# Kernel tuning notes

Hardware: AMD Instinct MI355X
Metric: run time of the kernel (lower is better)

## Reference

```python
import jax, jax.numpy as jnp
import numpy as np

DIM = 512
HEADS = 8
DIM_HEAD = 64
INNER = HEADS * DIM_HEAD  # 512
TOPK_FRAC = 0.7
SCALE = DIM_HEAD ** -0.5


def setup_inputs() -> dict:
    key = jax.random.key(0)
    k1, k2, k3, k4 = jax.random.split(key, 4)
    B, N = 4, 1024
    x = jax.random.normal(k1, (B, N, DIM), dtype=jnp.float32)
    # nn.Linear(dim, inner*3, bias=False): weight [3*inner, dim]; store transposed for x @ W
    w_qkv = jax.random.normal(k2, (DIM, 3 * INNER), dtype=jnp.float32) * (DIM ** -0.5)
    # to_out Linear(inner, dim) with bias
    w_out = jax.random.normal(k3, (INNER, DIM), dtype=jnp.float32) * (INNER ** -0.5)
    b_out = jax.random.normal(k4, (DIM,), dtype=jnp.float32) * 0.01
    return {"x": x, "w_qkv": w_qkv, "w_out": w_out, "b_out": b_out}


def reference(x, w_qkv, w_out, b_out):
    B, N, _ = x.shape
    H, D = HEADS, DIM_HEAD
    qkv = x @ w_qkv  # [B, N, 3*INNER]
    q, k, v = jnp.split(qkv, 3, axis=-1)
    # 'b n (h d) -> b h n d'
    reshape = lambda t: t.reshape(B, N, H, D).transpose(0, 2, 1, 3)
    q, k, v = reshape(q), reshape(k), reshape(v)
    dots = jnp.einsum('bhid,bhjd->bhij', q, k) * SCALE  # [B, H, N, N]
    # per-row top-k masking (kNN attention)
    kk = int(N * TOPK_FRAC)
    _, idx = jax.lax.top_k(dots, kk)  # [B, H, N, kk]
    bi = jnp.arange(B)[:, None, None, None]
    hi = jnp.arange(H)[None, :, None, None]
    ii = jnp.arange(N)[None, None, :, None]
    mask = jnp.zeros_like(dots).at[bi, hi, ii, idx].set(1.0)
    dots = jnp.where(mask > 0, dots, jnp.float32(-jnp.inf))
    attn = jax.nn.softmax(dots, axis=-1)
    out = jnp.einsum('bhij,bhjd->bhid', attn, v)  # [B, H, N, D]
    out = out.transpose(0, 2, 1, 3).reshape(B, N, H * D)  # 'b h n d -> b n (h d)'
    return out @ w_out + b_out
```

## Files before the change

### kernel.cpp

```cpp
#include <hip/hip_runtime.h>
#include <cstddef>

#define B_      4
#define N_      1024
#define DIM_    512
#define H_      8
#define D_      64
#define INNER_  512
#define TRIPLE_ 1536
#define KK_     716
#define SCALE_  0.125f

typedef short bf16x8 __attribute__((ext_vector_type(8)));
typedef float f32x4  __attribute__((ext_vector_type(4)));
typedef unsigned short ushort_t;
typedef ushort_t us8 __attribute__((ext_vector_type(8)));

__device__ __forceinline__ unsigned short bf16_rne(float f) {
    unsigned u = __float_as_uint(f);
    return (unsigned short)((u + 0x7FFFu + ((u >> 16) & 1u)) >> 16);
}
__device__ __forceinline__ float bf16_f(unsigned short s) {
    return __uint_as_float((unsigned)s << 16);
}
__device__ __forceinline__ unsigned f2key(float f) {
    unsigned u = __float_as_uint(f);
    return u ^ ((u & 0x80000000u) ? 0xFFFFFFFFu : 0x80000000u);
}
__device__ __forceinline__ float key2f(unsigned k) {
    unsigned u = (k & 0x80000000u) ? (k ^ 0x80000000u) : ~k;
    return __uint_as_float(u);
}
__device__ __forceinline__ int wave_count(int lc) {
    int c = __popcll(__ballot(lc & 1));
    c += __popcll(__ballot(lc & 2)) << 1;
    c += __popcll(__ballot(lc & 4)) << 2;
    c += __popcll(__ballot(lc & 8)) << 3;
    c += __popcll(__ballot(lc & 16)) << 4;
    return c;
}
__device__ __forceinline__ int count_ge(const unsigned* key, unsigned kt) {
    int lc = 0;
#pragma unroll
    for (int m = 0; m < 16; ++m) lc += (key[m] >= kt) ? 1 : 0;
    return wave_count(lc);
}
__device__ __forceinline__ unsigned bisect_exact(const unsigned* key,
                                                 bool hlo, bool hhi,
                                                 float tlo, float thi) {
    unsigned klo = hlo ? f2key(tlo) : 0u;
    unsigned khi = hhi ? f2key(thi) : 0xFFFFFFFFu;
    while (khi - klo > 1u) {
        const unsigned km = klo + ((khi - klo) >> 1);
        const int c = count_ge(key, km);
        if (c >= KK_) { klo = km; if (c == KK_) break; }
        else khi = km;
    }
    return klo;
}
__device__ __forceinline__ void topk2(const unsigned* key0, const unsigned* key1,
                                      float mu0, float sg0, float mu1, float sg1,
                                      unsigned& out0, unsigned& out1) {
    bool done0 = false, done1 = false;
    float tlo0 = 0.f, thi0 = 0.f, tlo1 = 0.f, thi1 = 0.f;
    int   clo0 = 0,   chi0 = 0,   clo1 = 0,   chi1 = 0;
    bool  hlo0 = false, hhi0 = false, hlo1 = false, hhi1 = false;
    float t0 = mu0 - 0.52189f * sg0;
    float t1 = mu1 - 0.52189f * sg1;
    unsigned res0 = 0u, res1 = 0u;
    for (int it = 0; it < 10; ++it) {
        if (done0 & done1) break;
        const unsigned kt0 = f2key(t0);
        const unsigned kt1 = f2key(t1);
        int lc0 = 0, lc1 = 0;
#pragma unroll
        for (int m = 0; m < 16; ++m) {
            lc0 += (key0[m] >= kt0) ? 1 : 0;
            lc1 += (key1[m] >= kt1) ? 1 : 0;
        }
        const int c0 = wave_count(lc0);
        const int c1 = wave_count(lc1);
        if (!done0) {
            if (c0 == KK_) { res0 = kt0; done0 = true; }
            else {
                if (c0 > KK_) { tlo0 = t0; clo0 = c0; hlo0 = true; }
                else          { thi0 = t0; chi0 = c0; hhi0 = true; }
                float tn;
                if (hlo0 && hhi0) {
                    tn = tlo0 + (thi0 - tlo0) * ((float)(clo0 - KK_) / (float)(clo0 - chi0));
                } else {
                    const float z    = (t0 - mu0) / sg0;
                    const float dens = fmaxf(408.5f * __expf(-0.5f * z * z) / sg0, 1.f);
                    tn = t0 + (float)(c0 - KK_) / dens;
                }
                if (hlo0 && !(tn > tlo0)) tn = hhi0 ? 0.5f * (tlo0 + thi0) : tlo0 + 0.25f * sg0;
                if (hhi0 && !(tn < thi0)) tn = hlo0 ? 0.5f * (tlo0 + thi0) : thi0 - 0.25f * sg0;
                t0 = tn;
            }
        }
        if (!done1) {
            if (c1 == KK_) { res1 = kt1; done1 = true; }
            else {
                if (c1 > KK_) { tlo1 = t1; clo1 = c1; hlo1 = true; }
                else          { thi1 = t1; chi1 = c1; hhi1 = true; }
                float tn;
                if (hlo1 && hhi1) {
                    tn = tlo1 + (thi1 - tlo1) * ((float)(clo1 - KK_) / (float)(clo1 - chi1));
                } else {
                    const float z    = (t1 - mu1) / sg1;
                    const float dens = fmaxf(408.5f * __expf(-0.5f * z * z) / sg1, 1.f);
                    tn = t1 + (float)(c1 - KK_) / dens;
                }
                if (hlo1 && !(tn > tlo1)) tn = hhi1 ? 0.5f * (tlo1 + thi1) : tlo1 + 0.25f * sg1;
                if (hhi1 && !(tn < thi1)) tn = hlo1 ? 0.5f * (tlo1 + thi1) : thi1 - 0.25f * sg1;
                t1 = tn;
            }
        }
    }
    if (!done0) res0 = bisect_exact(key0, hlo0, hhi0, tlo0, thi0);
    if (!done1) res1 = bisect_exact(key1, hlo1, hhi1, tlo1, thi1);
    out0 = res0;
    out1 = res1;
}
__device__ __forceinline__ void split8(const float* __restrict__ src,
                                       bf16x8& h8, bf16x8& l8) {
    float4 a = *(const float4*)src;
    float4 b = *(const float4*)(src + 4);
    float v[8] = {a.x, a.y, a.z, a.w, b.x, b.y, b.z, b.w};
#pragma unroll
    for (int i = 0; i < 8; ++i) {
        ushort_t hb = bf16_rne(v[i]);
        h8[i] = (short)hb;
        l8[i] = (short)bf16_rne(v[i] - bf16_f(hb));
    }
}

__global__ __launch_bounds__(256) void conv_wT2(const float* __restrict__ Wq,
                                                const float* __restrict__ Wo,
                                                ushort_t* __restrict__ WqTh,
                                                ushort_t* __restrict__ WqTl,
                                                ushort_t* __restrict__ WoTh,
                                                ushort_t* __restrict__ WoTl) {
    __shared__ float tile[32][33];
    const bool isQ = blockIdx.x < 48;
    const int  nb  = (isQ ? blockIdx.x : blockIdx.x - 48) * 32;
    const int  kb  = blockIdx.y * 32;
    const int  Nn  = isQ ? TRIPLE_ : DIM_;
    const float* W = isQ ? Wq : Wo;
    ushort_t* Th   = isQ ? WqTh : WoTh;
    ushort_t* Tl   = isQ ? WqTl : WoTl;
    const int tx = threadIdx.x & 31, ty = threadIdx.x >> 5;
    for (int yy = ty; yy < 32; yy += 8)
        tile[yy][tx] = W[(size_t)(kb + yy) * Nn + nb + tx];
    __syncthreads();
    for (int yy = ty; yy < 32; yy += 8) {
        float v = tile[tx][yy];
        ushort_t hb = bf16_rne(v);
        size_t idx = (size_t)(nb + yy) * DIM_ + kb + tx;
        Th[idx] = hb;
        Tl[idx] = bf16_rne(v - bf16_f(hb));
    }
}

__global__ __launch_bounds__(256) void gemm_qkv_mfma(
    const float* __restrict__ X,
    const ushort_t* __restrict__ Wh, const ushort_t* __restrict__ Wl,
    ushort_t* __restrict__ Qh, ushort_t* __restrict__ Ql,
    ushort_t* __restrict__ Kh, ushort_t* __restrict__ Kl,
    ushort_t* __restrict__ Vt) {
    __shared__ ushort_t stile[4][4608];
    __shared__ ushort_t BshH[2][2048];
    __shared__ ushort_t BshL[2][2048];
    const int t = threadIdx.x, w = t >> 6, l = t & 63;
    const int ln = l & 15, quad = l >> 4;
    const int n0 = blockIdx.y * 64;
    const int m0 = blockIdx.x * 128 + w * 32;
    f32x4 acc[2][4] = {};
    {
        const size_t xrow0 = (size_t)(m0 + ln) * DIM_;
        const size_t xrow1 = (size_t)(m0 + 16 + ln) * DIM_;
        const int srow = t >> 2;
        const int sk   = (t & 3) << 3;
        const size_t gb = (size_t)(n0 + srow) * DIM_ + sk;
        us8 nh = *(const us8*)&Wh[gb];
        us8 nl = *(const us8*)&Wl[gb];
        *(us8*)&BshH[0][t * 8] = nh;
        *(us8*)&BshL[0][t * 8] = nl;
        int cur = 0;
        for (int k0 = 0; k0 < DIM_; k0 += 32) {
            const bool more = (k0 + 32) < DIM_;
            const size_t gnext = gb + (size_t)(more ? k0 + 32 : 0);
            nh = *(const us8*)&Wh[gnext];
            nl = *(const us8*)&Wl[gnext];
            __syncthreads();
            const int ko = k0 + quad * 8;
            bf16x8 ah0, al0, ah1, al1;
            split8(&X[xrow0 + ko], ah0, al0);
            split8(&X[xrow1 + ko], ah1, al1);
#pragma unroll
            for (int j = 0; j < 4; ++j) {
                const int slot = (((j << 4) + ln) << 5) + (quad << 3);
                bf16x8 bh = *(const bf16x8*)&BshH[cur][slot];
                bf16x8 bl = *(const bf16x8*)&BshL[cur][slot];
                acc[0][j] = __builtin_amdgcn_mfma_f32_16x16x32_bf16(ah0, bh, acc[0][j], 0, 0, 0);
                acc[0][j] = __builtin_amdgcn_mfma_f32_16x16x32_bf16(al0, bh, acc[0][j], 0, 0, 0);
                acc[0][j] = __builtin_amdgcn_mfma_f32_16x16x32_bf16(ah0, bl, acc[0][j], 0, 0, 0);
                acc[1][j] = __builtin_amdgcn_mfma_f32_16x16x32_bf16(ah1, bh, acc[1][j], 0, 0, 0);
                acc[1][j] = __builtin_amdgcn_mfma_f32_16x16x32_bf16(al1, bh, acc[1][j], 0, 0, 0);
                acc[1][j] = __builtin_amdgcn_mfma_f32_16x16x32_bf16(ah1, bl, acc[1][j], 0, 0, 0);
            }
            if (more) {
                *(us8*)&BshH[cur ^ 1][t * 8] = nh;
                *(us8*)&BshL[cur ^ 1][t * 8] = nl;
            }
            cur ^= 1;
        }
    }
    const int sec = n0 >> 9;
    const int h   = (n0 >> 6) & 7;
    ushort_t* tw  = stile[w];
    const int b = m0 >> 10, nnb = m0 & 1023;
    if (sec < 2) {
        ushort_t* Hp = sec ? Kh : Qh;
        ushort_t* Lp = sec ? Kl : Ql;
        const float qsc = sec ? 1.0f : SCALE_;
#pragma unroll
        for (int i = 0; i < 2; ++i)
#pragma unroll
            for (int j = 0; j < 4; ++j)
#pragma unroll
                for (int g = 0; g < 4; ++g) {
                    const float v = acc[i][j][g] * qsc;
                    const ushort_t hb = bf16_rne(v);
                    const ushort_t lb = bf16_rne(v - bf16_f(hb));
                    const int tok = i * 16 + quad * 4 + g;
                    const int d   = j * 16 + ln;
                    tw[tok * 72 + d]        = hb;
                    tw[2304 + tok * 72 + d] = lb;
                }
        __syncthreads();
        const size_t rowbase = ((size_t)(b * 8 + h) * 1024 + nnb) * 64;
        const int dd = (l & 7) * 8;
#pragma unroll
        for (int s = 0; s < 4; ++s) {
            const int tl = s * 8 + (l >> 3);
            const size_t off = rowbase + (size_t)tl * 64 + dd;
            *(us8*)&Hp[off] = *(const us8*)&tw[tl * 72 + dd];
            *(us8*)&Lp[off] = *(const us8*)&tw[2304 + tl * 72 + dd];
        }
    } else {
#pragma unroll
        for (int i = 0; i < 2; ++i)
#pragma unroll
            for (int j = 0; j < 4; ++j)
#pragma unroll
                for (int g = 0; g < 4; ++g)
                    tw[(j * 16 + ln) * 40 + i * 16 + quad * 4 + g] = bf16_rne(acc[i][j][g]);
        __syncthreads();
        const size_t vbase = (size_t)(b * 8 + h) * 65536 + nnb;
#pragma unroll
        for (int p = 0; p < 2; ++p) {
            const int d = (p << 5) + (l >> 1);
            const int c = (l & 1) << 4;
            ushort_t* dst = &Vt[vbase + (size_t)d * 1024 + c];
            *(us8*)dst       = *(const us8*)&tw[d * 40 + c];
            *(us8*)(dst + 8) = *(const us8*)&tw[d * 40 + c + 8];
        }
    }
}

__global__ __launch_bounds__(256) void gemm_out_mfma(
    const ushort_t* __restrict__ Ah, const ushort_t* __restrict__ Al,
    const ushort_t* __restrict__ Wh, const ushort_t* __restrict__ Wl,
    const float* __restrict__ bias, float* __restrict__ C) {
    __shared__ ushort_t BshH[2][2048];
    __shared__ ushort_t BshL[2][2048];
    const int t = threadIdx.x, w = t >> 6, l = t & 63;
    const int ln = l & 15, quad = l >> 4;
    const int n0 = blockIdx.y * 64;
    const int m0 = blockIdx.x * 128 + w * 32;
    f32x4 acc[2][4] = {};
    {
        const size_t arow0 = (size_t)(m0 + ln) * INNER_;
        const size_t arow1 = (size_t)(m0 + 16 + ln) * INNER_;
        const int srow = t >> 2;
        const int sk   = (t & 3) << 3;
        const size_t gb = (size_t)(n0 + srow) * INNER_ + sk;
        us8 nh = *(const us8*)&Wh[gb];
        us8 nl = *(const us8*)&Wl[gb];
        *(us8*)&BshH[0][t * 8] = nh;
        *(us8*)&BshL[0][t * 8] = nl;
        int cur = 0;
        for (int k0 = 0; k0 < INNER_; k0 += 32) {
            const bool more = (k0 + 32) < INNER_;
            const size_t gnext = gb + (size_t)(more ? k0 + 32 : 0);
            nh = *(const us8*)&Wh[gnext];
            nl = *(const us8*)&Wl[gnext];
            __syncthreads();
            const int ko = k0 + quad * 8;
            bf16x8 ah0 = *(const bf16x8*)&Ah[arow0 + ko];
            bf16x8 al0 = *(const bf16x8*)&Al[arow0 + ko];
            bf16x8 ah1 = *(const bf16x8*)&Ah[arow1 + ko];
            bf16x8 al1 = *(const bf16x8*)&Al[arow1 + ko];
#pragma unroll
            for (int j = 0; j < 4; ++j) {
                const int slot = (((j << 4) + ln) << 5) + (quad << 3);
                bf16x8 bh = *(const bf16x8*)&BshH[cur][slot];
                bf16x8 bl = *(const bf16x8*)&BshL[cur][slot];
                acc[0][j] = __builtin_amdgcn_mfma_f32_16x16x32_bf16(ah0, bh, acc[0][j], 0, 0, 0);
                acc[0][j] = __builtin_amdgcn_mfma_f32_16x16x32_bf16(al0, bh, acc[0][j], 0, 0, 0);
                acc[0][j] = __builtin_amdgcn_mfma_f32_16x16x32_bf16(ah0, bl, acc[0][j], 0, 0, 0);
                acc[1][j] = __builtin_amdgcn_mfma_f32_16x16x32_bf16(ah1, bh, acc[1][j], 0, 0, 0);
                acc[1][j] = __builtin_amdgcn_mfma_f32_16x16x32_bf16(al1, bh, acc[1][j], 0, 0, 0);
                acc[1][j] = __builtin_amdgcn_mfma_f32_16x16x32_bf16(ah1, bl, acc[1][j], 0, 0, 0);
            }
            if (more) {
                *(us8*)&BshH[cur ^ 1][t * 8] = nh;
                *(us8*)&BshL[cur ^ 1][t * 8] = nl;
            }
            cur ^= 1;
        }
    }
#pragma unroll
    for (int i = 0; i < 2; ++i)
#pragma unroll
        for (int j = 0; j < 4; ++j) {
            const int col = n0 + j * 16 + ln;
            const float bb = bias[col];
#pragma unroll
            for (int g = 0; g < 4; ++g) {
                const int token = m0 + i * 16 + quad * 4 + g;
                C[(size_t)token * DIM_ + col] = acc[i][j][g] + bb;
            }
        }
}

__global__ __launch_bounds__(512)
__attribute__((amdgpu_waves_per_eu(4, 4)))
void attn_mfma(const ushort_t* __restrict__ Qh,
               const ushort_t* __restrict__ Ql,
               const ushort_t* __restrict__ Kh,
               const ushort_t* __restrict__ Kl,
               const ushort_t* __restrict__ Vt,
               ushort_t* __restrict__ Oh,
               ushort_t* __restrict__ Ol) {
    __shared__ float sdots[16 * 1024];
    __shared__ float spartial[4][16][17];

    const int t    = threadIdx.x;
    const int w    = t >> 6;
    const int l    = t & 63;
    const int ln   = l & 15;
    const int quad = l >> 4;
    const int wg   = blockIdx.x;
    const int bh   = wg & 31;
    const int i0   = (wg >> 5) << 4;

    const size_t bhoff = (size_t)bh << 16;

    const ushort_t* qp  = Qh + bhoff + (size_t)(i0 + ln) * 64 + (quad << 3);
    const ushort_t* qlp = Ql + bhoff + (size_t)(i0 + ln) * 64 + (quad << 3);
    bf16x8 qh0 = *(const bf16x8*)qp;
    bf16x8 qh1 = *(const bf16x8*)(qp + 32);
    bf16x8 ql0 = *(const bf16x8*)qlp;
    bf16x8 ql1 = *(const bf16x8*)(qlp + 32);

    const int dblk  = w & 3;
    const int jbase = (w & 4) << 7;
    const ushort_t* vp =
        Vt + bhoff + (size_t)((dblk << 4) + ln) * 1024 + (quad << 3) + jbase;
    bf16x8 vpre[8];

    for (int tt = 0; tt < 8; ++tt) {
        const int j0 = ((w << 3) + tt) << 4;
        const ushort_t* kp  = Kh + bhoff + (size_t)(j0 + ln) * 64 + (quad << 3);
        const ushort_t* klp = Kl + bhoff + (size_t)(j0 + ln) * 64 + (quad << 3);
        bf16x8 kh0 = *(const bf16x8*)kp;
        bf16x8 kh1 = *(const bf16x8*)(kp + 32);
        bf16x8 kl0 = *(const bf16x8*)klp;
        bf16x8 kl1 = *(const bf16x8*)(klp + 32);
        f32x4 acc = {0.f, 0.f, 0.f, 0.f};
        acc = __builtin_amdgcn_mfma_f32_16x16x32_bf16(qh0, kh0, acc, 0, 0, 0);
        acc = __builtin_amdgcn_mfma_f32_16x16x32_bf16(qh1, kh1, acc, 0, 0, 0);
        acc = __builtin_amdgcn_mfma_f32_16x16x32_bf16(qh0, kl0, acc, 0, 0, 0);
        acc = __builtin_amdgcn_mfma_f32_16x16x32_bf16(qh1, kl1, acc, 0, 0, 0);
        acc = __builtin_amdgcn_mfma_f32_16x16x32_bf16(ql0, kh0, acc, 0, 0, 0);
        acc = __builtin_amdgcn_mfma_f32_16x16x32_bf16(ql1, kh1, acc, 0, 0, 0);
#pragma unroll
        for (int g = 0; g < 4; ++g) {
            const int row = (quad << 2) + g;
            sdots[(row << 10) + ((j0 + ln) ^ ((row & 7) << 2))] = acc[g];
        }
    }
    __syncthreads();

    ushort_t* sP = (ushort_t*)sdots;
    {
        const int r0 = w << 1, r1 = r0 | 1;
        const int swz0 = (r0 & 7) << 2, swz1 = (r1 & 7) << 2;
        const float* s0 = &sdots[r0 << 10];
        const float* s1 = &sdots[r1 << 10];
        unsigned key0[16], key1[16];
        float sa0 = 0.f, sb0 = 0.f, sa1 = 0.f, sb1 = 0.f;
#pragma unroll
        for (int m = 0; m < 4; ++m) {
            f32x4 kv0 = *(const f32x4*)&s0[((l << 2) + (m << 8)) ^ swz0];
            f32x4 kv1 = *(const f32x4*)&s1[((l << 2) + (m << 8)) ^ swz1];
#pragma unroll
            for (int i = 0; i < 4; ++i) {
                key0[(m << 2) + i] = f2key(kv0[i]);
                key1[(m << 2) + i] = f2key(kv1[i]);
                sa0 += kv0[i];
                sb0 += kv0[i] * kv0[i];
                sa1 += kv1[i];
                sb1 += kv1[i] * kv1[i];
            }
        }
#pragma unroll
        for (int off = 32; off; off >>= 1) {
            sa0 += __shfl_xor(sa0, off, 64);
            sb0 += __shfl_xor(sb0, off, 64);
            sa1 += __shfl_xor(sa1, off, 64);
            sb1 += __shfl_xor(sb1, off, 64);
        }
        const float mu0 = sa0 * (1.0f / 1024.f);
        const float sg0 = sqrtf(fmaxf(sb0 * (1.0f / 1024.f) - mu0 * mu0, 1e-20f));
        const float mu1 = sa1 * (1.0f / 1024.f);
        const float sg1 = sqrtf(fmaxf(sb1 * (1.0f / 1024.f) - mu1 * mu1, 1e-20f));

        unsigned res0, res1;
        topk2(key0, key1, mu0, sg0, mu1, sg1, res0, res1);

        const float thr0 = key2f(res0), thr1 = key2f(res1);
        float pv0[16], pv1[16];
        float ls0 = 0.f, ls1 = 0.f;
#pragma unroll
        for (int m = 0; m < 16; ++m) {
            float p0 = (key0[m] >= res0) ? __expf(key2f(key0[m]) - thr0) : 0.f;
            float p1 = (key1[m] >= res1) ? __expf(key2f(key1[m]) - thr1) : 0.f;
            pv0[m] = p0;
            pv1[m] = p1;
            ls0 += p0;
            ls1 += p1;
        }
#pragma unroll
        for (int p = 0; p < 8; ++p)
            vpre[p] = *(const bf16x8*)(vp + p * 32);
#pragma unroll
        for (int off = 32; off; off >>= 1) {
            ls0 += __shfl_xor(ls0, off, 64);
            ls1 += __shfl_xor(ls1, off, 64);
        }
        const float inv0 = 1.f / ls0, inv1 = 1.f / ls1;
#pragma unroll
        for (int m = 0; m < 4; ++m) {
            const int g0 = ((l >> 1) + (m << 5)) ^ (r0 & 7);
            const int g1 = ((l >> 1) + (m << 5)) ^ (r1 & 7);
            ushort4 pk0 = make_ushort4(bf16_rne(pv0[(m << 2) + 0] * inv0),
                                       bf16_rne(pv0[(m << 2) + 1] * inv0),
                                       bf16_rne(pv0[(m << 2) + 2] * inv0),
                                       bf16_rne(pv0[(m << 2) + 3] * inv0));
            ushort4 pk1 = make_ushort4(bf16_rne(pv1[(m << 2) + 0] * inv1),
                                       bf16_rne(pv1[(m << 2) + 1] * inv1),
                                       bf16_rne(pv1[(m << 2) + 2] * inv1),
                                       bf16_rne(pv1[(m << 2) + 3] * inv1));
            *(ushort4*)&sP[(r0 << 11) + (g0 << 3) + ((l & 1) << 2)] = pk0;
            *(ushort4*)&sP[(r1 << 11) + (g1 << 3) + ((l & 1) << 2)] = pk1;
        }
    }
    __syncthreads();

    const int prow = ln << 11;
    const int rsw  = ln & 7;
    bf16x8 vnx[8];
#pragma unroll
    for (int p = 0; p < 8; ++p)
        vnx[p] = *(const bf16x8*)(vp + 256 + p * 32);
    f32x4 oa[4] = {};
    __builtin_amdgcn_s_setprio(1);
#pragma unroll
    for (int p = 0; p < 8; ++p) {
        const int j0 = p * 32;
        const int g = ((jbase + j0) >> 3) + quad;
        bf16x8 af = *(const bf16x8*)&sP[prow + ((g ^ rsw) << 3)];
        oa[p & 3] = __builtin_amdgcn_mfma_f32_16x16x32_bf16(af, vpre[p], oa[p & 3], 0, 0, 0);
    }
#pragma unroll
    for (int p = 0; p < 8; ++p) {
        const int j0 = 256 + p * 32;
        const int g = ((jbase + j0) >> 3) + quad;
        bf16x8 af = *(const bf16x8*)&sP[prow + ((g ^ rsw) << 3)];
        oa[p & 3] = __builtin_amdgcn_mfma_f32_16x16x32_bf16(af, vnx[p], oa[p & 3], 0, 0, 0);
    }
    __builtin_amdgcn_s_setprio(0);
    f32x4 oacc = (oa[0] + oa[1]) + (oa[2] + oa[3]);

    if (w & 4) {
#pragma unroll
        for (int g = 0; g < 4; ++g)
            spartial[dblk][(quad << 2) + g][ln] = oacc[g];
    }
    __syncthreads();
    if (!(w & 4)) {
        const int b = bh >> 3, h = bh & 7;
        const size_t obase =
            ((size_t)(b << 10) + i0 + (quad << 2)) * 512 + (h << 6) + (dblk << 4) + ln;
#pragma unroll
        for (int g = 0; g < 4; ++g) {
            const float v = oacc[g] + spartial[dblk][(quad << 2) + g][ln];
            ushort_t hb = bf16_rne(v);
            Oh[obase + (size_t)g * 512] = hb;
            Ol[obase + (size_t)g * 512] = bf16_rne(v - bf16_f(hb));
        }
    }
}

extern "C" void kernel_launch(void* const* d_in, const int* in_sizes, int n_in,
                              void* d_out, int out_size, void* d_ws, size_t ws_size,
                              hipStream_t stream) {
    const float* x     = (const float*)d_in[0];
    const float* w_qkv = (const float*)d_in[1];
    const float* w_out = (const float*)d_in[2];
    const float* b_out = (const float*)d_in[3];
    float*       out   = (float*)d_out;

    const size_t ON  = (size_t)4096 * 512;
    const size_t WQT = (size_t)1536 * 512;
    const size_t WOT = (size_t)512 * 512;
    const size_t QK  = (size_t)32 * 1024 * 64;

    ushort_t* p    = (ushort_t*)d_ws;
    ushort_t* Oh   = p;            p += ON;
    ushort_t* Ol   = p;            p += ON;
    ushort_t* WqTh = p;            p += WQT;
    ushort_t* WqTl = p;            p += WQT;
    ushort_t* WoTh = p;            p += WOT;
    ushort_t* WoTl = p;            p += WOT;
    ushort_t* Qh   = p;            p += QK;
    ushort_t* Ql   = p;            p += QK;
    ushort_t* Kh   = p;            p += QK;
    ushort_t* Kl   = p;            p += QK;
    ushort_t* Vt   = p;            p += QK;

    conv_wT2<<<dim3(64, 16), 256, 0, stream>>>(w_qkv, w_out, WqTh, WqTl, WoTh, WoTl);

    gemm_qkv_mfma<<<dim3(4096 / 128, TRIPLE_ / 64), 256, 0, stream>>>(
        x, WqTh, WqTl, Qh, Ql, Kh, Kl, Vt);

    attn_mfma<<<dim3(B_ * H_ * (N_ / 16)), 512, 0, stream>>>(Qh, Ql, Kh, Kl, Vt, Oh, Ol);

    gemm_out_mfma<<<dim3(4096 / 128, DIM_ / 64), 256, 0, stream>>>(
        Oh, Ol, WoTh, WoTl, b_out, out);
}
```

Before: 222.7 us.

## Pre-split X to bf16 hi/lo and enlarge QKV GEMM M-tile per wave

Adds a split_x kernel that converts X into bf16 high/low halves once, stored in the O workspace buffers, instead of splitting inside every QKV GEMM block. The QKV GEMM now reads the pre-split bf16 operands and each wave computes 64 rows instead of 32, doubling reuse of each B fragment loaded from LDS and halving the grid. The epilogue is done in two halves with extra barriers. This costs an extra kernel launch and a round trip through global memory for Xh/Xl, raises register pressure (hence launch_bounds 256,3), and leaves fewer blocks to fill the CUs.

```diff
diff --git a/kernel.cpp b/kernel.cpp
--- a/kernel.cpp
+++ b/kernel.cpp
@@ -133,6 +133,16 @@
         h8[i] = (short)hb;
         l8[i] = (short)bf16_rne(v[i] - bf16_f(hb));
     }
+}
+
+__global__ __launch_bounds__(256) void split_x(const float* __restrict__ X,
+                                               ushort_t* __restrict__ Xh,
+                                               ushort_t* __restrict__ Xl) {
+    const int idx = (blockIdx.x * 256 + threadIdx.x) * 8;
+    bf16x8 h8, l8;
+    split8(&X[idx], h8, l8);
+    *(bf16x8*)&Xh[idx] = h8;
+    *(bf16x8*)&Xl[idx] = l8;
 }
 
 __global__ __launch_bounds__(256) void conv_wT2(const float* __restrict__ Wq,
@@ -162,8 +172,8 @@
     }
 }
 
-__global__ __launch_bounds__(256) void gemm_qkv_mfma(
-    const float* __restrict__ X,
+__global__ __launch_bounds__(256, 3) void gemm_qkv_mfma(
+    const ushort_t* __restrict__ Ah, const ushort_t* __restrict__ Al,
     const ushort_t* __restrict__ Wh, const ushort_t* __restrict__ Wl,
     ushort_t* __restrict__ Qh, ushort_t* __restrict__ Ql,
     ushort_t* __restrict__ Kh, ushort_t* __restrict__ Kl,
@@ -174,11 +184,13 @@
     const int t = threadIdx.x, w = t >> 6, l = t & 63;
     const int ln = l & 15, quad = l >> 4;
     const int n0 = blockIdx.y * 64;
-    const int m0 = blockIdx.x * 128 + w * 32;
-    f32x4 acc[2][4] = {};
+    const int m0w = blockIdx.x * 256 + w * 64;
+    f32x4 acc[4][4] = {};
     {
-        const size_t xrow0 = (size_t)(m0 + ln) * DIM_;
-        const size_t xrow1 = (size_t)(m0 + 16 + ln) * DIM_;
+        size_t arow[4];
+#pragma unroll
+        for (int i = 0; i < 4; ++i)
+            arow[i] = (size_t)(m0w + i * 16 + ln) * DIM_;
         const int srow = t >> 2;
         const int sk   = (t & 3) << 3;
         const size_t gb = (size_t)(n0 + srow) * DIM_ + sk;
@@ -193,21 +205,24 @@
             nh = *(const us8*)&Wh[gnext];
             nl = *(const us8*)&Wl[gnext];
             __syncthreads();
-            const int ko = k0 + quad * 8;
-            bf16x8 ah0, al0, ah1, al1;
-            split8(&X[xrow0 + ko], ah0, al0);
-            split8(&X[xrow1 + ko], ah1, al1);
+            const int ko = k0 + (quad << 3);
+            bf16x8 ah[4], al[4];
+#pragma unroll
+            for (int i = 0; i < 4; ++i) {
+                ah[i] = *(const bf16x8*)&Ah[arow[i] + ko];
+                al[i] = *(const bf16x8*)&Al[arow[i] + ko];
+            }
 #pragma unroll
             for (int j = 0; j < 4; ++j) {
                 const int slot = (((j << 4) + ln) << 5) + (quad << 3);
                 bf16x8 bh = *(const bf16x8*)&BshH[cur][slot];
                 bf16x8 bl = *(const bf16x8*)&BshL[cur][slot];
-                acc[0][j] = __builtin_amdgcn_mfma_f32_16x16x32_bf16(ah0, bh, acc[0][j], 0, 0, 0);
-                acc[0][j] = __builtin_amdgcn_mfma_f32_16x16x32_bf16(al0, bh, acc[0][j], 0, 0, 0);
-                acc[0][j] = __builtin_amdgcn_mfma_f32_16x16x32_bf16(ah0, bl, acc[0][j], 0, 0, 0);
-                acc[1][j] = __builtin_amdgcn_mfma_f32_16x16x32_bf16(ah1, bh, acc[1][j], 0, 0, 0);
-                acc[1][j] = __builtin_amdgcn_mfma_f32_16x16x32_bf16(al1, bh, acc[1][j], 0, 0, 0);
-                acc[1][j] = __builtin_amdgcn_mfma_f32_16x16x32_bf16(ah1, bl, acc[1][j], 0, 0, 0);
+#pragma unroll
+                for (int i = 0; i < 4; ++i) {
+                    acc[i][j] = __builtin_amdgcn_mfma_f32_16x16x32_bf16(ah[i], bh, acc[i][j], 0, 0, 0);
+                    acc[i][j] = __builtin_amdgcn_mfma_f32_16x16x32_bf16(al[i], bh, acc[i][j], 0, 0, 0);
+                    acc[i][j] = __builtin_amdgcn_mfma_f32_16x16x32_bf16(ah[i], bl, acc[i][j], 0, 0, 0);
+                }
             }
             if (more) {
                 *(us8*)&BshH[cur ^ 1][t * 8] = nh;
@@ -219,52 +234,67 @@
     const int sec = n0 >> 9;
     const int h   = (n0 >> 6) & 7;
     ushort_t* tw  = stile[w];
-    const int b = m0 >> 10, nnb = m0 & 1023;
     if (sec < 2) {
         ushort_t* Hp = sec ? Kh : Qh;
         ushort_t* Lp = sec ? Kl : Ql;
         const float qsc = sec ? 1.0f : SCALE_;
 #pragma unroll
-        for (int i = 0; i < 2; ++i)
-#pragma unroll
-            for (int j = 0; j < 4; ++j)
-#pragma unroll
-                for (int g = 0; g < 4; ++g) {
-                    const float v = acc[i][j][g] * qsc;
-                    const ushort_t hb = bf16_rne(v);
-                    const ushort_t lb = bf16_rne(v - bf16_f(hb));
-                    const int tok = i * 16 + quad * 4 + g;
-                    const int d   = j * 16 + ln;
-                    tw[tok * 72 + d]        = hb;
-                    tw[2304 + tok * 72 + d] = lb;
-                }
-        __syncthreads();
-        const size_t rowbase = ((size_t)(b * 8 + h) * 1024 + nnb) * 64;
-        const int dd = (l & 7) * 8;
-#pragma unroll
-        for (int s = 0; s < 4; ++s) {
-            const int tl = s * 8 + (l >> 3);
-            const size_t off = rowbase + (size_t)tl * 64 + dd;
-            *(us8*)&Hp[off] = *(const us8*)&tw[tl * 72 + dd];
-            *(us8*)&Lp[off] = *(const us8*)&tw[2304 + tl * 72 + dd];
+        for (int half = 0; half < 2; ++half) {
+#pragma unroll
+            for (int i2 = 0; i2 < 2; ++i2) {
+                const int i = half * 2 + i2;
+#pragma unroll
+                for (int j = 0; j < 4; ++j)
+#pragma unroll
+                    for (int g = 0; g < 4; ++g) {
+                        const float v = acc[i][j][g] * qsc;
+                        const ushort_t hb = bf16_rne(v);
+                        const ushort_t lb = bf16_rne(v - bf16_f(hb));
+                        const int tok = i2 * 16 + quad * 4 + g;
+                        const int d   = j * 16 + ln;
+                        tw[tok * 72 + d]        = hb;
+                        tw[2304 + tok * 72 + d] = lb;
+                    }
+            }
+            __syncthreads();
+            const int mbase = m0w + half * 32;
+            const int b = mbase >> 10, nnb = mbase & 1023;
+            const size_t rowbase = ((size_t)(b * 8 + h) * 1024 + nnb) * 64;
+            const int dd = (l & 7) * 8;
+#pragma unroll
+            for (int s = 0; s < 4; ++s) {
+                const int tl = s * 8 + (l >> 3);
+                const size_t off = rowbase + (size_t)tl * 64 + dd;
+                *(us8*)&Hp[off] = *(const us8*)&tw[tl * 72 + dd];
+                *(us8*)&Lp[off] = *(const us8*)&tw[2304 + tl * 72 + dd];
+            }
+            __syncthreads();
         }
     } else {
 #pragma unroll
-        for (int i = 0; i < 2; ++i)
-#pragma unroll
-            for (int j = 0; j < 4; ++j)
-#pragma unroll
-                for (int g = 0; g < 4; ++g)
-                    tw[(j * 16 + ln) * 40 + i * 16 + quad * 4 + g] = bf16_rne(acc[i][j][g]);
-        __syncthreads();
-        const size_t vbase = (size_t)(b * 8 + h) * 65536 + nnb;
-#pragma unroll
-        for (int p = 0; p < 2; ++p) {
-            const int d = (p << 5) + (l >> 1);
-            const int c = (l & 1) << 4;
-            ushort_t* dst = &Vt[vbase + (size_t)d * 1024 + c];
-            *(us8*)dst       = *(const us8*)&tw[d * 40 + c];
-            *(us8*)(dst + 8) = *(const us8*)&tw[d * 40 + c + 8];
+        for (int half = 0; half < 2; ++half) {
+#pragma unroll
+            for (int i2 = 0; i2 < 2; ++i2) {
+                const int i = half * 2 + i2;
+#pragma unroll
+                for (int j = 0; j < 4; ++j)
+#pragma unroll
+                    for (int g = 0; g < 4; ++g)
+                        tw[(j * 16 + ln) * 40 + i2 * 16 + quad * 4 + g] = bf16_rne(acc[i][j][g]);
+            }
+            __syncthreads();
+            const int mbase = m0w + half * 32;
+            const int b = mbase >> 10, nnb = mbase & 1023;
+            const size_t vbase = (size_t)(b * 8 + h) * 65536 + nnb;
+#pragma unroll
+            for (int p = 0; p < 2; ++p) {
+                const int d = (p << 5) + (l >> 1);
+                const int c = (l & 1) << 4;
+                ushort_t* dst = &Vt[vbase + (size_t)d * 1024 + c];
+                *(us8*)dst       = *(const us8*)&tw[d * 40 + c];
+                *(us8*)(dst + 8) = *(const us8*)&tw[d * 40 + c + 8];
+            }
+            __syncthreads();
         }
     }
 }
@@ -542,10 +572,15 @@
     ushort_t* Kl   = p;            p += QK;
     ushort_t* Vt   = p;            p += QK;
 
+    ushort_t* Xh = Oh;
+    ushort_t* Xl = Ol;
+
+    split_x<<<dim3((4096 * 512 / 8) / 256), 256, 0, stream>>>(x, Xh, Xl);
+
     conv_wT2<<<dim3(64, 16), 256, 0, stream>>>(w_qkv, w_out, WqTh, WqTl, WoTh, WoTl);
 
-    gemm_qkv_mfma<<<dim3(4096 / 128, TRIPLE_ / 64), 256, 0, stream>>>(
-        x, WqTh, WqTl, Qh, Ql, Kh, Kl, Vt);
+    gemm_qkv_mfma<<<dim3(4096 / 256, TRIPLE_ / 64), 256, 0, stream>>>(
+        Xh, Xl, WqTh, WqTl, Qh, Ql, Kh, Kl, Vt);
 
     attn_mfma<<<dim3(B_ * H_ * (N_ / 16)), 512, 0, stream>>>(Qh, Ql, Kh, Kl, Vt, Oh, Ol);
 
```

Measured after the change: 232.7 us. 1.05x slower.
